# Kernel optimization log

Hardware: AMD Instinct MI355X
Metric: run time of the kernel (lower is better)

Reference implementation:

```python
import jax, jax.numpy as jnp
import numpy as np

OUT_H, OUT_W = 512, 512
BATCH, CHANNELS = 64, 3


def setup_inputs() -> dict:
    key = jax.random.key(0)
    k1, k2 = jax.random.split(key)
    U = jax.random.normal(k1, (BATCH, OUT_H, OUT_W, CHANNELS), dtype=jnp.float32)
    theta = jax.random.normal(k2, (BATCH, 1), dtype=jnp.float32)
    return {"U": U, "theta": theta}


def reference(U, theta):
    B = U.shape[0]
    H, W = OUT_H, OUT_W
    # normalized sampling grid [H*W, 3] with homogeneous coordinate
    gx, gy = jnp.meshgrid(jnp.linspace(-1.0, 1.0, W), jnp.linspace(-1.0, 1.0, H))
    grid = jnp.stack([gx, gy, jnp.ones_like(gx)], axis=-1).reshape(H * W, 3)
    # rotation-only affine matrix [B, 2, 3]
    cos_t, sin_t, z = jnp.cos(theta), jnp.sin(theta), jnp.zeros_like(theta)
    rot = jnp.concatenate([cos_t, -sin_t, z, sin_t, cos_t, z], axis=1).reshape(B, 2, 3)
    # transformed source coords [B, H*W, 2]
    T_g = jnp.einsum('bij,nj->bni', rot, grid)
    x = (T_g[..., 0] + 1.0) * (W - 1) / 2.0
    y = (T_g[..., 1] + 1.0) * (H - 1) / 2.0
    x0f = jnp.floor(x).astype(jnp.int32)
    y0f = jnp.floor(y).astype(jnp.int32)
    x0 = jnp.clip(x0f, 0, W - 1)
    x1 = jnp.clip(x0f + 1, 0, W - 1)
    y0 = jnp.clip(y0f, 0, H - 1)
    y1 = jnp.clip(y0f + 1, 0, H - 1)
    # 4-corner gathers, batched: [B, H*W, C]
    gather = jax.vmap(lambda u, yy, xx: u[yy, xx])
    Ia = gather(U, y0, x0)
    Ib = gather(U, y1, x0)
    Ic = gather(U, y0, x1)
    Id = gather(U, y1, x1)
    x0_f, x1_f = x0.astype(jnp.float32), x1.astype(jnp.float32)
    y0_f, y1_f = y0.astype(jnp.float32), y1.astype(jnp.float32)
    wa = (x1_f - x) * (y1_f - y)
    wb = (x1_f - x) * (y - y0_f)
    wc = (x - x0_f) * (y1_f - y)
    wd = (x - x0_f) * (y - y0_f)
    out = (wa[..., None] * Ia + wb[..., None] * Ib
           + wc[..., None] * Ic + wd[..., None] * Id)
    return out.reshape(B, H, W, -1)
```

## Files before the change

### kernel.cpp

```cpp
#include <hip/hip_runtime.h>
#include <hip/hip_fp16.h>

#define OUT_H 512
#define OUT_W 512
#define BATCH 64
#define CHANS 3

#define LROWS 47
#define LPITCH 49

__global__ __launch_bounds__(256) void st_bilinear_kernel(
    const float* __restrict__ U,
    const float* __restrict__ theta,
    float* __restrict__ out)
{
    __shared__ uint2 sm[LROWS * LPITCH + 1];

    int blk  = blockIdx.x;
    int lblk = (blk & 7) * 2048 + (blk >> 3);

    int b  = lblk >> 8;
    int t  = lblk & 255;
    int i0 = (t >> 4) << 5;
    int j0 = (t & 15) << 5;

    int tid = threadIdx.x;

    float tt = theta[b];
    float s, c;
    __sincosf(tt, &s, &c);

    const float scale = 2.0f / 511.0f;
    float gx0 = (float)j0 * scale - 1.0f;
    float gy0 = (float)i0 * scale - 1.0f;
    float xb0 = (c * gx0 - s * gy0 + 1.0f) * 255.5f;
    float yb0 = (s * gx0 + c * gy0 + 1.0f) * 255.5f;

    float xmin = xb0 + fminf(0.0f, 31.0f * c) + fminf(0.0f, -31.0f * s);
    float ymin = yb0 + fminf(0.0f, 31.0f * s) + fminf(0.0f,  31.0f * c);

    int bx0 = min(max((int)floorf(xmin), 0), OUT_W - 1);
    int by0 = min(max((int)floorf(ymin), 0), OUT_H - 1);
    int bx_load = min(bx0, OUT_W - 48);
    int by_load = min(by0, OUT_H - 46);

    const float* Ub = U + (size_t)b * (OUT_H * OUT_W * CHANS);
    const float* gb = Ub + ((size_t)by_load * OUT_W + bx_load) * CHANS;
    for (int u = tid; u < 46 * 48; u += 256) {
        int r  = u / 48;
        int px = u - r * 48;
        const float* p = gb + (size_t)r * (OUT_W * CHANS) + px * CHANS;
        float2 c01 = *(const float2*)p;
        float  c2  = p[2];
        __half2 h01 = __floats2half2_rn(c01.x, c01.y);
        __half2 h2  = __floats2half2_rn(c2, 0.0f);
        uint2 v;
        v.x = *(const unsigned int*)&h01;
        v.y = *(const unsigned int*)&h2;
        sm[r * LPITCH + px] = v;
    }
    __syncthreads();

    int il = tid >> 3;
    int jb = (tid & 7) << 2;
    float ilf = (float)il;
    float xr = xb0 - s * ilf;
    float yr = yb0 + c * ilf;

    float o[12];
#pragma unroll
    for (int p = 0; p < 4; ++p) {
        float jlf = (float)(jb + p);
        float x = fmaf(c, jlf, xr);
        float y = fmaf(s, jlf, yr);

        float x0f = floorf(x);
        float y0f = floorf(y);
        float fx = x - x0f;
        float fy = y - y0f;
        float hx = 1.0f - fx;
        float hy = 1.0f - fy;
        __half2 wa2 = __float2half2_rn(hx * hy);
        __half2 wb2 = __float2half2_rn(hx * fy);
        __half2 wc2 = __float2half2_rn(fx * hy);
        __half2 wd2 = __float2half2_rn(fx * fy);

        int lx = min(max((int)x0f - bx_load, 0), 48);
        int ly = min(max((int)y0f - by_load, 0), 45);
        int idx = ly * LPITCH + lx;

        uint2 rA = sm[idx];
        uint2 rC = sm[idx + 1];
        uint2 rB = sm[idx + LPITCH];
        uint2 rD = sm[idx + LPITCH + 1];

        __half2 a01 = *(const __half2*)&rA.x, a2 = *(const __half2*)&rA.y;
        __half2 c01 = *(const __half2*)&rC.x, c2 = *(const __half2*)&rC.y;
        __half2 b01 = *(const __half2*)&rB.x, b2 = *(const __half2*)&rB.y;
        __half2 d01 = *(const __half2*)&rD.x, d2 = *(const __half2*)&rD.y;

        __half2 r01 = __hmul2(wa2, a01);
        r01 = __hfma2(wb2, b01, r01);
        r01 = __hfma2(wc2, c01, r01);
        r01 = __hfma2(wd2, d01, r01);
        __half2 r2h = __hmul2(wa2, a2);
        r2h = __hfma2(wb2, b2, r2h);
        r2h = __hfma2(wc2, c2, r2h);
        r2h = __hfma2(wd2, d2, r2h);

        bool valid = (x >= 0.0f) && (x < 511.0f) && (y >= 0.0f) && (y < 511.0f);
        o[p * 3 + 0] = valid ? __low2float(r01)  : 0.0f;
        o[p * 3 + 1] = valid ? __high2float(r01) : 0.0f;
        o[p * 3 + 2] = valid ? __low2float(r2h)  : 0.0f;
    }

    float* po = out + (((size_t)b * OUT_H + (i0 + il)) * OUT_W + (j0 + jb)) * CHANS;
    ((float4*)po)[0] = make_float4(o[0], o[1], o[2],  o[3]);
    ((float4*)po)[1] = make_float4(o[4], o[5], o[6],  o[7]);
    ((float4*)po)[2] = make_float4(o[8], o[9], o[10], o[11]);
}

extern "C" void kernel_launch(void* const* d_in, const int* in_sizes, int n_in,
                              void* d_out, int out_size, void* d_ws, size_t ws_size,
                              hipStream_t stream) {
    const float* U     = (const float*)d_in[0];
    const float* theta = (const float*)d_in[1];
    float* out = (float*)d_out;

    int blocks = BATCH * (OUT_H / 32) * (OUT_W / 32);
    st_bilinear_kernel<<<blocks, 256, 0, stream>>>(U, theta, out);
}
```

Measured before the change: 117.3 us.

## Split LDS tile into planar halves with vectorized loads and lerp interpolation

```diff
diff --git a/kernel.cpp b/kernel.cpp
--- a/kernel.cpp
+++ b/kernel.cpp
@@ -6,15 +6,19 @@
 #define BATCH 64
 #define CHANS 3
 
-#define LROWS 47
-#define LPITCH 49
+#define WROWS 48
+#define WPX   48
+#define LPITCH 50
+#define LSLOTS (WROWS * LPITCH)
+#define IDX_MAX 2348
 
 __global__ __launch_bounds__(256) void st_bilinear_kernel(
     const float* __restrict__ U,
     const float* __restrict__ theta,
     float* __restrict__ out)
 {
-    __shared__ uint2 sm[LROWS * LPITCH + 1];
+    __shared__ __align__(16) unsigned int smA[LSLOTS];
+    __shared__ __align__(16) unsigned int smB[LSLOTS];
 
     int blk  = blockIdx.x;
     int lblk = (blk & 7) * 2048 + (blk >> 3);
@@ -41,23 +45,43 @@
 
     int bx0 = min(max((int)floorf(xmin), 0), OUT_W - 1);
     int by0 = min(max((int)floorf(ymin), 0), OUT_H - 1);
-    int bx_load = min(bx0, OUT_W - 48);
-    int by_load = min(by0, OUT_H - 46);
+    int bx_load = min(bx0, OUT_W - WPX);
+    int by_load = min(by0, OUT_H - WROWS);
 
     const float* Ub = U + (size_t)b * (OUT_H * OUT_W * CHANS);
     const float* gb = Ub + ((size_t)by_load * OUT_W + bx_load) * CHANS;
-    for (int u = tid; u < 46 * 48; u += 256) {
-        int r  = u / 48;
-        int px = u - r * 48;
-        const float* p = gb + (size_t)r * (OUT_W * CHANS) + px * CHANS;
-        float2 c01 = *(const float2*)p;
-        float  c2  = p[2];
-        __half2 h01 = __floats2half2_rn(c01.x, c01.y);
-        __half2 h2  = __floats2half2_rn(c2, 0.0f);
-        uint2 v;
-        v.x = *(const unsigned int*)&h01;
-        v.y = *(const unsigned int*)&h2;
-        sm[r * LPITCH + px] = v;
+
+    float4 va[5];
+    float2 vb[5];
+#pragma unroll
+    for (int it = 0; it < 5; ++it) {
+        unsigned P = (unsigned)tid + 256u * it;
+        if (it < 4 || tid < 128) {
+            unsigned r  = P / 24u;
+            unsigned pr = P - r * 24u;
+            const float* p = gb + (size_t)r * (OUT_W * CHANS) + pr * 6u;
+            va[it] = *(const float4*)p;
+            vb[it] = *(const float2*)(p + 4);
+        }
+    }
+#pragma unroll
+    for (int it = 0; it < 5; ++it) {
+        unsigned P = (unsigned)tid + 256u * it;
+        if (it < 4 || tid < 128) {
+            unsigned r  = P / 24u;
+            unsigned pr = P - r * 24u;
+            unsigned slot = r * LPITCH + pr * 2u;
+            float4 v = va[it]; float2 w = vb[it];
+            __half2 ha0 = __floats2half2_rn(v.x, v.y);
+            __half2 hb0 = __floats2half2_rn(v.z, 0.0f);
+            __half2 ha1 = __floats2half2_rn(v.w, w.x);
+            __half2 hb1 = __floats2half2_rn(w.y, 0.0f);
+            uint2 wa, wb;
+            wa.x = *(unsigned int*)&ha0; wa.y = *(unsigned int*)&ha1;
+            wb.x = *(unsigned int*)&hb0; wb.y = *(unsigned int*)&hb1;
+            *(uint2*)(smA + slot) = wa;
+            *(uint2*)(smB + slot) = wb;
+        }
     }
     __syncthreads();
 
@@ -66,6 +90,7 @@
     float ilf = (float)il;
     float xr = xb0 - s * ilf;
     float yr = yb0 + c * ilf;
+    int Koff = by_load * LPITCH + bx_load;
 
     float o[12];
 #pragma unroll
@@ -74,44 +99,37 @@
         float x = fmaf(c, jlf, xr);
         float y = fmaf(s, jlf, yr);
 
-        float x0f = floorf(x);
-        float y0f = floorf(y);
-        float fx = x - x0f;
-        float fy = y - y0f;
-        float hx = 1.0f - fx;
-        float hy = 1.0f - fy;
-        __half2 wa2 = __float2half2_rn(hx * hy);
-        __half2 wb2 = __float2half2_rn(hx * fy);
-        __half2 wc2 = __float2half2_rn(fx * hy);
-        __half2 wd2 = __float2half2_rn(fx * fy);
+        int ix = __float2int_rd(x);
+        int iy = __float2int_rd(y);
+        float fx = x - (float)ix;
+        float fy = y - (float)iy;
 
-        int lx = min(max((int)x0f - bx_load, 0), 48);
-        int ly = min(max((int)y0f - by_load, 0), 45);
-        int idx = ly * LPITCH + lx;
+        int idx = iy * LPITCH + ix - Koff;
+        idx = min(max(idx, 0), IDX_MAX);
 
-        uint2 rA = sm[idx];
-        uint2 rC = sm[idx + 1];
-        uint2 rB = sm[idx + LPITCH];
-        uint2 rD = sm[idx + LPITCH + 1];
+        unsigned iA0 = smA[idx],          iA1 = smA[idx + 1];
+        unsigned iA2 = smA[idx + LPITCH], iA3 = smA[idx + LPITCH + 1];
+        unsigned iB0 = smB[idx],          iB1 = smB[idx + 1];
+        unsigned iB2 = smB[idx + LPITCH], iB3 = smB[idx + LPITCH + 1];
 
-        __half2 a01 = *(const __half2*)&rA.x, a2 = *(const __half2*)&rA.y;
-        __half2 c01 = *(const __half2*)&rC.x, c2 = *(const __half2*)&rC.y;
-        __half2 b01 = *(const __half2*)&rB.x, b2 = *(const __half2*)&rB.y;
-        __half2 d01 = *(const __half2*)&rD.x, d2 = *(const __half2*)&rD.y;
+        __half2 fx2 = __float2half2_rn(fx);
+        __half2 fy2 = __float2half2_rn(fy);
+        __half2 A0 = *(__half2*)&iA0, A1 = *(__half2*)&iA1;
+        __half2 A2 = *(__half2*)&iA2, A3 = *(__half2*)&iA3;
+        __half2 B0 = *(__half2*)&iB0, B1 = *(__half2*)&iB1;
+        __half2 B2 = *(__half2*)&iB2, B3 = *(__half2*)&iB3;
 
-        __half2 r01 = __hmul2(wa2, a01);
-        r01 = __hfma2(wb2, b01, r01);
-        r01 = __hfma2(wc2, c01, r01);
-        r01 = __hfma2(wd2, d01, r01);
-        __half2 r2h = __hmul2(wa2, a2);
-        r2h = __hfma2(wb2, b2, r2h);
-        r2h = __hfma2(wc2, c2, r2h);
-        r2h = __hfma2(wd2, d2, r2h);
+        __half2 tA = __hfma2(fx2, __hsub2(A1, A0), A0);
+        __half2 bA = __hfma2(fx2, __hsub2(A3, A2), A2);
+        __half2 rA = __hfma2(fy2, __hsub2(bA, tA), tA);
+        __half2 tB = __hfma2(fx2, __hsub2(B1, B0), B0);
+        __half2 bB = __hfma2(fx2, __hsub2(B3, B2), B2);
+        __half2 rB = __hfma2(fy2, __hsub2(bB, tB), tB);
 
         bool valid = (x >= 0.0f) && (x < 511.0f) && (y >= 0.0f) && (y < 511.0f);
-        o[p * 3 + 0] = valid ? __low2float(r01)  : 0.0f;
-        o[p * 3 + 1] = valid ? __high2float(r01) : 0.0f;
-        o[p * 3 + 2] = valid ? __low2float(r2h)  : 0.0f;
+        o[p * 3 + 0] = valid ? __low2float(rA)  : 0.0f;
+        o[p * 3 + 1] = valid ? __high2float(rA) : 0.0f;
+        o[p * 3 + 2] = valid ? __low2float(rB)  : 0.0f;
     }
 
     float* po = out + (((size_t)b * OUT_H + (i0 + il)) * OUT_W + (j0 + jb)) * CHANS;
```

New measurement: 103.4 us. 11.9% less time.
